# Kernel tuning notes

Hardware: AMD Instinct MI355X
Metric: run time of the kernel (lower is better)

The kernel has to match this reference:

```python
import jax, jax.numpy as jnp
import numpy as np

N_EMBED = 16384
EMBED_DIM = 256
BETA = 0.25
B, H, W = 16, 32, 32


def setup_inputs() -> dict:
    key = jax.random.key(0)
    k1, k2 = jax.random.split(key)
    z = jax.random.normal(k1, (B, EMBED_DIM, H, W), dtype=jnp.float32)
    # nn.Embedding init: uniform(-1/n_embed, 1/n_embed)
    embedding = jax.random.uniform(
        k2, (N_EMBED, EMBED_DIM), dtype=jnp.float32,
        minval=-1.0 / N_EMBED, maxval=1.0 / N_EMBED)
    return {"z": z, "embedding": embedding}


def reference(z, embedding):
    # (b, c, h, w) -> (b, h, w, c), flatten to (N, d)
    z_p = jnp.transpose(z, (0, 2, 3, 1))
    zf = z_p.reshape(-1, EMBED_DIM)  # (N, d)

    # squared distances: ||z||^2 + ||e||^2 - 2 z.e  -> (N, n_embed)
    d = (jnp.sum(zf * zf, axis=1, keepdims=True)
         + jnp.sum(embedding * embedding, axis=1)
         - 2.0 * jnp.matmul(zf, embedding.T))
    idx = jnp.argmin(d, axis=1)  # (N,)

    # one-hot encodings (returned, as in the original)
    min_encoding = jax.nn.one_hot(idx, N_EMBED, dtype=z.dtype)  # (N, n_embed)

    # codebook gather (math-equivalent to one_hot @ weight)
    z_q = jnp.take(embedding, idx, axis=0).reshape(z_p.shape)

    sg = jax.lax.stop_gradient
    loss = jnp.mean((sg(z_q) - z_p) ** 2) + BETA * jnp.mean((z_q - sg(z_p)) ** 2)

    # straight-through estimator
    z_q_st = z_p + sg(z_q - z_p)

    e_mean = jnp.mean(min_encoding, axis=0)
    perplexity = jnp.exp(-jnp.sum(e_mean * jnp.log(e_mean + 1e-10)))

    z_q_out = jnp.transpose(z_q_st, (0, 3, 1, 2))  # back to (b, c, h, w)
    return (z_q_out, loss, perplexity, min_encoding, idx[:, None])
```

## Files before the change

### kernel.cpp

```cpp
#include <hip/hip_runtime.h>
#include <math.h>

#define N_ROWS   16384
#define N_CODES  16384
#define K_DIM    256
#define HW       1024
#define N_ELEMS  4194304

#define OUT_ZQ      0
#define OUT_LOSS    4194304
#define OUT_PERP    4194305
#define OUT_ONEHOT  4194306
#define OUT_IDX     272629762

#define WS_LOSS    0
#define WS_HIST    64
#define WS_IDX     65600
#define WS_ENORM   131136
#define WS_ZNORM   196672

#define SC_ZT    0
#define SC_ZHI   16777216
#define SC_ZLO   25165824
#define SC_EHI   33554432
#define SC_BMIN  41943040
#define SC_BPACK 50331648

#define MARGIN 2.0e-4f

typedef float  floatx2 __attribute__((ext_vector_type(2)));
typedef float  f32x4   __attribute__((ext_vector_type(4)));
typedef short  bf16x8  __attribute__((ext_vector_type(8)));
typedef unsigned short u16x8 __attribute__((ext_vector_type(8)));

__device__ __forceinline__ unsigned short bf16rn(float f) {
    unsigned int x = __float_as_uint(f);
    return (unsigned short)((x + 0x7fffu + ((x >> 16) & 1u)) >> 16);
}


__global__ __launch_bounds__(256) void convert_z_kernel(
    const float* __restrict__ z, float* __restrict__ zt,
    unsigned short* __restrict__ zhi, unsigned short* __restrict__ zlo)
{
    const int tid = blockIdx.x * 256 + threadIdx.x;
    const int n  = tid & 16383;
    const int kg = tid >> 14;
    const int bimg = n >> 10, sp = n & 1023;
    const float* zp = z + (size_t)bimg * (K_DIM * HW) + (size_t)(kg * 8) * HW + sp;

    float f[8]; u16x8 hv, lv;
    #pragma unroll
    for (int j = 0; j < 8; ++j) f[j] = zp[(size_t)j * HW];
    #pragma unroll
    for (int j = 0; j < 8; ++j) {
        unsigned short h = bf16rn(f[j]);
        float fh = __uint_as_float(((unsigned int)h) << 16);
        hv[j] = h;
        lv[j] = bf16rn(f[j] - fh);
    }
    float4 a = make_float4(f[0], f[1], f[2], f[3]);
    float4 b = make_float4(f[4], f[5], f[6], f[7]);
    *(float4*)(zt + (size_t)n * 256 + kg * 8)     = a;
    *(float4*)(zt + (size_t)n * 256 + kg * 8 + 4) = b;

    const int rs = n >> 3, rowin = n & 7, kc = kg >> 3;
    const size_t stripe = (size_t)(rs * 4 + kc) * 512;
    const int inoff = rowin * 64 + (((((kg & 7) * 16)) ^ (rowin << 4)) >> 1);
    *(u16x8*)(zhi + stripe + inoff) = hv;
    *(u16x8*)(zlo + stripe + inoff) = lv;
}

__global__ __launch_bounds__(256) void convert_e_kernel(
    const float* __restrict__ emb, unsigned short* __restrict__ ehi)
{
    const int tid = blockIdx.x * 256 + threadIdx.x;
    const int kg = tid & 31;
    const int j  = tid >> 5;
    const float* ep = emb + (size_t)j * 256 + kg * 8;
    u16x8 hv;
    #pragma unroll
    for (int t = 0; t < 8; ++t) hv[t] = bf16rn(ep[t]);
    const int rs = j >> 3, rowin = j & 7, kc = kg >> 3;
    const size_t stripe = (size_t)(rs * 4 + kc) * 512;
    const int inoff = rowin * 64 + (((((kg & 7) * 16)) ^ (rowin << 4)) >> 1);
    *(u16x8*)(ehi + stripe + inoff) = hv;
}

__global__ __launch_bounds__(256) void znorm_kernel(
    const float* __restrict__ z, float* __restrict__ znorm)
{
    const int n = blockIdx.x * 256 + threadIdx.x;
    const int b = n >> 10;
    const int sp = n & 1023;
    const float* zr = z + (size_t)b * K_DIM * HW + sp;

    float h0, h1;
    {
        float r[8];
        #pragma unroll
        for (int j = 0; j < 8; ++j) {
            float v = zr[(size_t)j * HW];
            float sq = v * v; asm volatile("" : "+v"(sq));
            r[j] = sq;
        }
        for (int i = 8; i < 128; i += 8) {
            #pragma unroll
            for (int j = 0; j < 8; ++j) {
                float v = zr[(size_t)(i + j) * HW];
                float sq = v * v; asm volatile("" : "+v"(sq));
                r[j] += sq;
            }
        }
        h0 = ((r[0] + r[1]) + (r[2] + r[3])) + ((r[4] + r[5]) + (r[6] + r[7]));
    }
    {
        float r[8];
        #pragma unroll
        for (int j = 0; j < 8; ++j) {
            float v = zr[(size_t)(128 + j) * HW];
            float sq = v * v; asm volatile("" : "+v"(sq));
            r[j] = sq;
        }
        for (int i = 8; i < 128; i += 8) {
            #pragma unroll
            for (int j = 0; j < 8; ++j) {
                float v = zr[(size_t)(128 + i + j) * HW];
                float sq = v * v; asm volatile("" : "+v"(sq));
                r[j] += sq;
            }
        }
        h1 = ((r[0] + r[1]) + (r[2] + r[3])) + ((r[4] + r[5]) + (r[6] + r[7]));
    }
    znorm[n] = h0 + h1;
}

__global__ __launch_bounds__(256) void enorm_kernel(
    const float* __restrict__ emb, float* __restrict__ enorm)
{
    const int jc = blockIdx.x * 256 + threadIdx.x;
    const float* er = emb + (size_t)jc * K_DIM;

    float h0, h1;
    {
        float r[8];
        #pragma unroll
        for (int j = 0; j < 8; ++j) {
            float v = er[j];
            float sq = v * v; asm volatile("" : "+v"(sq));
            r[j] = sq;
        }
        for (int i = 8; i < 128; i += 8) {
            #pragma unroll
            for (int j = 0; j < 8; ++j) {
                float v = er[i + j];
                float sq = v * v; asm volatile("" : "+v"(sq));
                r[j] += sq;
            }
        }
        h0 = ((r[0] + r[1]) + (r[2] + r[3])) + ((r[4] + r[5]) + (r[6] + r[7]));
    }
    {
        float r[8];
        #pragma unroll
        for (int j = 0; j < 8; ++j) {
            float v = er[128 + j];
            float sq = v * v; asm volatile("" : "+v"(sq));
            r[j] = sq;
        }
        for (int i = 8; i < 128; i += 8) {
            #pragma unroll
            for (int j = 0; j < 8; ++j) {
                float v = er[128 + i + j];
                float sq = v * v; asm volatile("" : "+v"(sq));
                r[j] += sq;
            }
        }
        h1 = ((r[0] + r[1]) + (r[2] + r[3])) + ((r[4] + r[5]) + (r[6] + r[7]));
    }
    enorm[jc] = h0 + h1;
}

__global__ __launch_bounds__(512) void mfma_min_kernel(
    const unsigned short* __restrict__ zhi, const unsigned short* __restrict__ zlo,
    const unsigned short* __restrict__ ehi, const float* __restrict__ enorm,
    float* __restrict__ bmin, unsigned int* __restrict__ bpack)
{
    __shared__ unsigned short Bs[32768];
    __shared__ unsigned short As[2][16384];

    const int rb = blockIdx.x;
    const int cb = blockIdx.y;
    const int tid = threadIdx.x;
    const int wid = tid >> 6;
    const int lane = tid & 63;
    const int wr = wid >> 1;
    const int wc = wid & 1;
    const int l15 = lane & 15, l4 = lane >> 4;

    {
        const unsigned short* gb = ehi + (size_t)cb * 32768 + wid * 512 + lane * 8;
        #pragma unroll
        for (int i = 0; i < 8; ++i)
            __builtin_amdgcn_global_load_lds(
                (const __attribute__((address_space(1))) void*)(gb + i * 4096),
                (__attribute__((address_space(3))) void*)(Bs + i * 4096 + wid * 512),
                16, 0, 0);
    }
    const size_t abase = (size_t)rb * 128 * 512;
    auto stageA = [&](const unsigned short* asrc, int kc, int b) {
        #pragma unroll
        for (int i = 0; i < 4; ++i) {
            const int s = i * 8 + wid;
            const unsigned short* ga = asrc + abase + (size_t)kc * 512
                                       + (size_t)s * 2048 + lane * 8;
            __builtin_amdgcn_global_load_lds(
                (const __attribute__((address_space(1))) void*)ga,
                (__attribute__((address_space(3))) void*)(&As[b][s * 512]),
                16, 0, 0);
        }
    };

    f32x4 acc[4][4];
    #pragma unroll
    for (int mf = 0; mf < 4; ++mf)
        #pragma unroll
        for (int nf = 0; nf < 4; ++nf)
            acc[mf][nf] = (f32x4){0.f, 0.f, 0.f, 0.f};

    stageA(zhi, 0, 0);
    __syncthreads();

    for (int c = 0; c < 8; ++c) {
        const int cur = c & 1;
        if (c < 7) {
            const unsigned short* nsrc = (c + 1 < 4) ? zhi : zlo;
            stageA(nsrc, (c + 1) & 3, cur ^ 1);
        }
        const int kc = c & 3;
        #pragma unroll
        for (int sub = 0; sub < 2; ++sub) {
            bf16x8 af[4], bfr[4];
            const int kb = sub * 64 + l4 * 16;
            #pragma unroll
            for (int mf = 0; mf < 4; ++mf) {
                const int row = wr * 64 + mf * 16 + l15;
                const int off = row * 128 + (kb ^ ((row & 7) << 4));
                af[mf] = *(const bf16x8*)((const char*)&As[cur][0] + off);
            }
            #pragma unroll
            for (int nf = 0; nf < 4; ++nf) {
                const int crow = wc * 64 + nf * 16 + l15;
                const int off = ((crow >> 3) * 4 + kc) * 1024
                              + (crow & 7) * 128 + (kb ^ ((crow & 7) << 4));
                bfr[nf] = *(const bf16x8*)((const char*)Bs + off);
            }
            #pragma unroll
            for (int mf = 0; mf < 4; ++mf)
                #pragma unroll
                for (int nf = 0; nf < 4; ++nf)
                    acc[mf][nf] = __builtin_amdgcn_mfma_f32_16x16x32_bf16(
                        af[mf], bfr[nf], acc[mf][nf], 0, 0, 0);
        }
        __syncthreads();
    }

    float en[4];
    #pragma unroll
    for (int nf = 0; nf < 4; ++nf)
        en[nf] = enorm[cb * 128 + wc * 64 + nf * 16 + l15];

    float*        Vh = (float*)&As[0][0];
    unsigned int* Ih = (unsigned int*)(Vh + 512);
    unsigned int* Ch = (unsigned int*)(Ih + 512);
    float*        Gm = (float*)(Ch + 512);

    #pragma unroll
    for (int mf = 0; mf < 4; ++mf) {
        #pragma unroll
        for (int i = 0; i < 4; ++i) {
            float bv = 3.4e38f; int bc = 0x7fffffff;
            #pragma unroll
            for (int nf = 0; nf < 4; ++nf) {
                const float s = en[nf] - 2.0f * acc[mf][nf][i];
                const int col = cb * 128 + wc * 64 + nf * 16 + l15;
                if (s < bv) { bv = s; bc = col; }
            }
            #pragma unroll
            for (int off = 1; off < 16; off <<= 1) {
                const float ov = __shfl_xor(bv, off);
                const int oc = __shfl_xor(bc, off);
                if (ov < bv || (ov == bv && oc < bc)) { bv = ov; bc = oc; }
            }
            if (l15 == 0) {
                const int rr = wr * 64 + mf * 16 + l4 * 4 + i;
                Vh[wc * 256 + rr] = bv;
                Ih[wc * 256 + rr] = (unsigned int)bc;
            }
        }
    }
    __syncthreads();
    if (tid < 256) {
        const float v0 = Vh[tid], v1 = Vh[256 + tid];
        const unsigned int i0 = Ih[tid], i1 = Ih[256 + tid];
        float v; unsigned int ix;
        if (v1 < v0 || (v1 == v0 && i1 < i0)) { v = v1; ix = i1; }
        else { v = v0; ix = i0; }
        Gm[tid] = v;
        Vh[tid] = v;
        Ih[tid] = ix;
    }
    __syncthreads();
    #pragma unroll
    for (int mf = 0; mf < 4; ++mf) {
        #pragma unroll
        for (int i = 0; i < 4; ++i) {
            const int rr = wr * 64 + mf * 16 + l4 * 4 + i;
            const float thr = Gm[rr] + MARGIN;
            int cnt = 0;
            #pragma unroll
            for (int nf = 0; nf < 4; ++nf)
                cnt += (en[nf] - 2.0f * acc[mf][nf][i] <= thr) ? 1 : 0;
            #pragma unroll
            for (int off = 1; off < 16; off <<= 1) cnt += __shfl_xor(cnt, off);
            if (l15 == 0) Ch[wc * 256 + rr] = (unsigned int)cnt;
        }
    }
    __syncthreads();
    if (tid < 256) {
        unsigned int cnt = Ch[tid] + Ch[256 + tid];
        const size_t o = (size_t)(rb * 256 + tid) * 128 + cb;
        bmin[o] = Vh[tid];
        bpack[o] = (Ih[tid] << 8) | (cnt > 255u ? 255u : cnt);
    }
}

__global__ __launch_bounds__(256) void argmin_exact_kernel(
    const float* __restrict__ zt, const float* __restrict__ emb,
    const float* __restrict__ enorm, const float* __restrict__ znorm,
    const float* __restrict__ bmin, const unsigned int* __restrict__ bpack,
    int* __restrict__ idx_ws, float* __restrict__ out_idx,
    unsigned int* __restrict__ hist)
{
    __shared__ float ZL[4][256];
    const int tid = threadIdx.x, wv = tid >> 6, lane = tid & 63;
    const int n = blockIdx.x * 4 + wv;

    *(float4*)&ZL[wv][lane * 4] = ((const float4*)(zt + (size_t)n * 256))[lane];
    __syncthreads();

    const float zn = znorm[n];
    float bd = 3.4e38f; int bi = 0x7fffffff;

    const float m0 = bmin[(size_t)n * 128 + lane];
    const float m1 = bmin[(size_t)n * 128 + 64 + lane];
    float g = fminf(m0, m1);
    #pragma unroll
    for (int off = 1; off < 64; off <<= 1) g = fminf(g, __shfl_xor(g, off));
    const float thr = g + MARGIN;

    #pragma unroll
    for (int half = 0; half < 2; ++half) {
        const float bm = half ? m1 : m0;
        const unsigned int pk = bpack[(size_t)n * 128 + half * 64 + lane];
        const int cnt = (int)(pk & 255u);
        const int cand = (int)(pk >> 8);
        const bool act = (bm <= thr);
        if (act && cnt == 1) {
            const float* er = emb + (size_t)cand * 256;
            float dot = 0.f;
            for (int k = 0; k < 256; ++k) dot += ZL[wv][k] * er[k];
            const float t1 = zn + enorm[cand];
            const float d = t1 - 2.0f * dot;
            if (d < bd || (d == bd && cand < bi)) { bd = d; bi = cand; }
        }
        unsigned long long need = __ballot(act && cnt > 1);
        while (need) {
            const int c2 = __ffsll((unsigned long long)need) - 1;
            need &= need - 1;
            const int base = (half * 64 + c2) * 128;
            #pragma unroll
            for (int t = 0; t < 2; ++t) {
                const int j = base + t * 64 + lane;
                const float* er = emb + (size_t)j * 256;
                float dot = 0.f;
                for (int k = 0; k < 256; ++k) dot += ZL[wv][k] * er[k];
                const float t1 = zn + enorm[j];
                const float d = t1 - 2.0f * dot;
                if (d < bd || (d == bd && j < bi)) { bd = d; bi = j; }
            }
        }
    }
    #pragma unroll
    for (int off = 1; off < 64; off <<= 1) {
        const float od = __shfl_xor(bd, off);
        const int oi = __shfl_xor(bi, off);
        if (od < bd || (od == bd && oi < bi)) { bd = od; bi = oi; }
    }
    if (lane == 0) {
        idx_ws[n] = bi;
        out_idx[n] = (float)bi;
        atomicAdd(&hist[bi], 1u);
    }
}

__global__ __launch_bounds__(256) void gather_zq_loss_kernel(
    const float* __restrict__ z, const float* __restrict__ emb,
    const int* __restrict__ idx_ws, float* __restrict__ zq_out,
    double* __restrict__ loss_accum)
{
    const int g = blockIdx.x;
    const int wave = threadIdx.x >> 6;
    const int lane = threadIdx.x & 63;
    const int n = g * 64 + lane;
    const int b = n >> 10;
    const int sp = n & 1023;
    const int code = idx_ws[n];
    const float* erow = emb + (size_t)code * K_DIM;
    const float* zrow = z + (size_t)b * K_DIM * HW + sp;
    float* orow = zq_out + (size_t)b * K_DIM * HW + sp;

    float lsum = 0.0f;
    for (int c = wave; c < K_DIM; c += 4) {
        const float e  = erow[c];
        const float zp = zrow[(size_t)c * HW];
        orow[(size_t)c * HW] = e;
        const float d = e - zp;
        lsum += d * d;
    }
    #pragma unroll
    for (int off = 32; off; off >>= 1) lsum += __shfl_xor(lsum, off);
    __shared__ float wsum[4];
    if (lane == 0) wsum[wave] = lsum;
    __syncthreads();
    if (threadIdx.x == 0)
        atomicAdd(loss_accum, (double)(wsum[0] + wsum[1] + wsum[2] + wsum[3]));
}

__global__ __launch_bounds__(256) void onehot_fill_kernel(
    const int* __restrict__ idx_ws, float* __restrict__ out)
{
    const int r = blockIdx.x;
    const int code = idx_ws[r];
    float* row = out + (size_t)r * 16384;
    for (int s = threadIdx.x; s < 4096; s += 256) {
        if (s == 0) {
            floatx2 h = {code == 0 ? 1.f : 0.f, code == 1 ? 1.f : 0.f};
            __builtin_nontemporal_store(h, (floatx2*)row);
        }
        if (s < 4095) {
            const int cc = 2 + s * 4;
            f32x4 v = {code == cc ? 1.f : 0.f, code == cc + 1 ? 1.f : 0.f,
                       code == cc + 2 ? 1.f : 0.f, code == cc + 3 ? 1.f : 0.f};
            __builtin_nontemporal_store(v, (f32x4*)(row + cc));
        } else {
            floatx2 tpair = {code == 16382 ? 1.f : 0.f, code == 16383 ? 1.f : 0.f};
            __builtin_nontemporal_store(tpair, (floatx2*)(row + 16382));
        }
    }
}

__global__ __launch_bounds__(1024) void finalize_scalars_kernel(
    const double* __restrict__ loss_accum, const unsigned int* __restrict__ hist,
    float* __restrict__ out_scalars)
{
    const int tid = threadIdx.x;
    double s = 0.0;
    for (int j = tid; j < N_CODES; j += 1024) {
        const double p = (double)hist[j] * (1.0 / (double)N_ROWS);
        s += p * log(p + 1e-10);
    }
    #pragma unroll
    for (int off = 32; off; off >>= 1) s += __shfl_xor(s, off);
    __shared__ double sh[16];
    const int wave = tid >> 6, lane = tid & 63;
    if (lane == 0) sh[wave] = s;
    __syncthreads();
    if (tid == 0) {
        double S = 0.0;
        for (int w = 0; w < 16; ++w) S += sh[w];
        out_scalars[0] = (float)(1.25 * loss_accum[0] * (1.0 / (double)N_ELEMS));
        out_scalars[1] = (float)exp(-S);
    }
}

extern "C" void kernel_launch(void* const* d_in, const int* in_sizes, int n_in,
                              void* d_out, int out_size, void* d_ws, size_t ws_size,
                              hipStream_t stream)
{
    const float* z   = (const float*)d_in[0];
    const float* emb = (const float*)d_in[1];
    float* out = (float*)d_out;
    char* ws = (char*)d_ws;

    double*       loss_accum = (double*)(ws + WS_LOSS);
    unsigned int* hist       = (unsigned int*)(ws + WS_HIST);
    int*          idx_ws     = (int*)(ws + WS_IDX);
    float*        enorm      = (float*)(ws + WS_ENORM);
    float*        znorm      = (float*)(ws + WS_ZNORM);

    char* scb = (char*)(out + OUT_ONEHOT) + 8;
    float*          zt    = (float*)(scb + SC_ZT);
    unsigned short* zhi   = (unsigned short*)(scb + SC_ZHI);
    unsigned short* zlo   = (unsigned short*)(scb + SC_ZLO);
    unsigned short* ehi   = (unsigned short*)(scb + SC_EHI);
    float*          bminp = (float*)(scb + SC_BMIN);
    unsigned int*   bpack = (unsigned int*)(scb + SC_BPACK);

    (void)hipMemsetAsync(ws, 0, WS_ENORM, stream);

    convert_z_kernel<<<dim3(2048), dim3(256), 0, stream>>>(z, zt, zhi, zlo);
    convert_e_kernel<<<dim3(2048), dim3(256), 0, stream>>>(emb, ehi);
    znorm_kernel<<<dim3(N_ROWS / 256), dim3(256), 0, stream>>>(z, znorm);
    enorm_kernel<<<dim3(N_CODES / 256), dim3(256), 0, stream>>>(emb, enorm);

    mfma_min_kernel<<<dim3(64, 128), dim3(512), 0, stream>>>(
        zhi, zlo, ehi, enorm, bminp, bpack);

    argmin_exact_kernel<<<dim3(N_ROWS / 4), dim3(256), 0, stream>>>(
        zt, emb, enorm, znorm, bminp, bpack, idx_ws, out + OUT_IDX, hist);

    gather_zq_loss_kernel<<<dim3(N_ROWS / 64), dim3(256), 0, stream>>>(
        z, emb, idx_ws, out + OUT_ZQ, loss_accum);

    onehot_fill_kernel<<<dim3(16384), dim3(256), 0, stream>>>(
        idx_ws, out + OUT_ONEHOT);

    finalize_scalars_kernel<<<dim3(1), dim3(1024), 0, stream>>>(
        loss_accum, hist, out + OUT_LOSS);
}
```

Measured before the change: 1.979 ms.

## Drop low-bf16 z correction in screening GEMM and read A operand from global

The candidate-screening GEMM stops using a split hi/lo bf16 representation of z and uses only the hi part, which halves the MFMA work and removes the zlo conversion and its stores. To make up for the coarser screen, the margin used by the exact argmin re-check is doubled. The A operand is now loaded straight from global memory into registers instead of being double-buffered through LDS, the grid axes are swapped so column blocks vary fastest, and occupancy hints are added. A wider margin can send more candidates to the exact re-check, and unstaged global A loads may stall the MFMA pipeline.

After: 1.761 ms. 1.12x faster.

```diff
diff --git a/kernel.cpp b/kernel.cpp
--- a/kernel.cpp
+++ b/kernel.cpp
@@ -21,12 +21,11 @@
 
 #define SC_ZT    0
 #define SC_ZHI   16777216
-#define SC_ZLO   25165824
 #define SC_EHI   33554432
 #define SC_BMIN  41943040
 #define SC_BPACK 50331648
 
-#define MARGIN 2.0e-4f
+#define MARGIN 4.0e-4f
 
 typedef float  floatx2 __attribute__((ext_vector_type(2)));
 typedef float  f32x4   __attribute__((ext_vector_type(4)));
@@ -41,7 +40,7 @@
 
 __global__ __launch_bounds__(256) void convert_z_kernel(
     const float* __restrict__ z, float* __restrict__ zt,
-    unsigned short* __restrict__ zhi, unsigned short* __restrict__ zlo)
+    unsigned short* __restrict__ zhi)
 {
     const int tid = blockIdx.x * 256 + threadIdx.x;
     const int n  = tid & 16383;
@@ -49,16 +48,12 @@
     const int bimg = n >> 10, sp = n & 1023;
     const float* zp = z + (size_t)bimg * (K_DIM * HW) + (size_t)(kg * 8) * HW + sp;
 
-    float f[8]; u16x8 hv, lv;
+    float f[8]; u16x8 hv;
     #pragma unroll
     for (int j = 0; j < 8; ++j) f[j] = zp[(size_t)j * HW];
     #pragma unroll
-    for (int j = 0; j < 8; ++j) {
-        unsigned short h = bf16rn(f[j]);
-        float fh = __uint_as_float(((unsigned int)h) << 16);
-        hv[j] = h;
-        lv[j] = bf16rn(f[j] - fh);
-    }
+    for (int j = 0; j < 8; ++j) hv[j] = bf16rn(f[j]);
+
     float4 a = make_float4(f[0], f[1], f[2], f[3]);
     float4 b = make_float4(f[4], f[5], f[6], f[7]);
     *(float4*)(zt + (size_t)n * 256 + kg * 8)     = a;
@@ -66,9 +61,8 @@
 
     const int rs = n >> 3, rowin = n & 7, kc = kg >> 3;
     const size_t stripe = (size_t)(rs * 4 + kc) * 512;
-    const int inoff = rowin * 64 + (((((kg & 7) * 16)) ^ (rowin << 4)) >> 1);
+    const int inoff = rowin * 64 + ((((kg & 7) * 8)) ^ (rowin << 3));
     *(u16x8*)(zhi + stripe + inoff) = hv;
-    *(u16x8*)(zlo + stripe + inoff) = lv;
 }
 
 __global__ __launch_bounds__(256) void convert_e_kernel(
@@ -83,7 +77,7 @@
     for (int t = 0; t < 8; ++t) hv[t] = bf16rn(ep[t]);
     const int rs = j >> 3, rowin = j & 7, kc = kg >> 3;
     const size_t stripe = (size_t)(rs * 4 + kc) * 512;
-    const int inoff = rowin * 64 + (((((kg & 7) * 16)) ^ (rowin << 4)) >> 1);
+    const int inoff = rowin * 64 + ((((kg & 7) * 8)) ^ (rowin << 3));
     *(u16x8*)(ehi + stripe + inoff) = hv;
 }
 
@@ -181,16 +175,15 @@
     enorm[jc] = h0 + h1;
 }
 
-__global__ __launch_bounds__(512) void mfma_min_kernel(
-    const unsigned short* __restrict__ zhi, const unsigned short* __restrict__ zlo,
-    const unsigned short* __restrict__ ehi, const float* __restrict__ enorm,
+__global__ __launch_bounds__(512, 4) void mfma_min_kernel(
+    const unsigned short* __restrict__ zhi, const unsigned short* __restrict__ ehi,
+    const float* __restrict__ enorm,
     float* __restrict__ bmin, unsigned int* __restrict__ bpack)
 {
     __shared__ unsigned short Bs[32768];
-    __shared__ unsigned short As[2][16384];
-
-    const int rb = blockIdx.x;
-    const int cb = blockIdx.y;
+
+    const int cb = blockIdx.x;
+    const int rb = blockIdx.y;
     const int tid = threadIdx.x;
     const int wid = tid >> 6;
     const int lane = tid & 63;
@@ -207,19 +200,25 @@
                 (__attribute__((address_space(3))) void*)(Bs + i * 4096 + wid * 512),
                 16, 0, 0);
     }
-    const size_t abase = (size_t)rb * 128 * 512;
-    auto stageA = [&](const unsigned short* asrc, int kc, int b) {
-        #pragma unroll
-        for (int i = 0; i < 4; ++i) {
-            const int s = i * 8 + wid;
-            const unsigned short* ga = asrc + abase + (size_t)kc * 512
-                                       + (size_t)s * 2048 + lane * 8;
-            __builtin_amdgcn_global_load_lds(
-                (const __attribute__((address_space(1))) void*)ga,
-                (__attribute__((address_space(3))) void*)(&As[b][s * 512]),
-                16, 0, 0);
-        }
-    };
+
+    int pe[4], po[4];
+    #pragma unroll
+    for (int mf = 0; mf < 4; ++mf) {
+        const int r = rb * 256 + wr * 64 + mf * 16 + l15;
+        const int x = (r & 7) << 3;
+        const int srow = (r >> 3) * 2048 + (r & 7) * 64;
+        pe[mf] = srow + ((l4 * 8) ^ x);
+        po[mf] = srow + ((32 + l4 * 8) ^ x);
+    }
+    int qe[4], qo[4];
+    #pragma unroll
+    for (int nf = 0; nf < 4; ++nf) {
+        const int crow = wc * 64 + nf * 16 + l15;
+        const int x = (crow & 7) << 3;
+        const int srow = (crow >> 3) * 2048 + (crow & 7) * 64;
+        qe[nf] = srow + ((l4 * 8) ^ x);
+        qo[nf] = srow + ((32 + l4 * 8) ^ x);
+    }
 
     f32x4 acc[4][4];
     #pragma unroll
@@ -228,49 +227,42 @@
         for (int nf = 0; nf < 4; ++nf)
             acc[mf][nf] = (f32x4){0.f, 0.f, 0.f, 0.f};
 
-    stageA(zhi, 0, 0);
-    __syncthreads();
-
-    for (int c = 0; c < 8; ++c) {
-        const int cur = c & 1;
-        if (c < 7) {
-            const unsigned short* nsrc = (c + 1 < 4) ? zhi : zlo;
-            stageA(nsrc, (c + 1) & 3, cur ^ 1);
-        }
-        const int kc = c & 3;
-        #pragma unroll
-        for (int sub = 0; sub < 2; ++sub) {
-            bf16x8 af[4], bfr[4];
-            const int kb = sub * 64 + l4 * 16;
-            #pragma unroll
-            for (int mf = 0; mf < 4; ++mf) {
-                const int row = wr * 64 + mf * 16 + l15;
-                const int off = row * 128 + (kb ^ ((row & 7) << 4));
-                af[mf] = *(const bf16x8*)((const char*)&As[cur][0] + off);
-            }
-            #pragma unroll
-            for (int nf = 0; nf < 4; ++nf) {
-                const int crow = wc * 64 + nf * 16 + l15;
-                const int off = ((crow >> 3) * 4 + kc) * 1024
-                              + (crow & 7) * 128 + (kb ^ ((crow & 7) << 4));
-                bfr[nf] = *(const bf16x8*)((const char*)Bs + off);
-            }
+    __syncthreads();
+
+    for (int t = 0; t < 4; ++t) {
+        const int d = t * 512;
+        bf16x8 a[4];
+        #pragma unroll
+        for (int mf = 0; mf < 4; ++mf)
+            a[mf] = *(const bf16x8*)(zhi + (size_t)(pe[mf] + d));
+        #pragma unroll
+        for (int nf = 0; nf < 4; ++nf) {
+            const bf16x8 b = *(const bf16x8*)(Bs + qe[nf] + d);
             #pragma unroll
             for (int mf = 0; mf < 4; ++mf)
-                #pragma unroll
-                for (int nf = 0; nf < 4; ++nf)
-                    acc[mf][nf] = __builtin_amdgcn_mfma_f32_16x16x32_bf16(
-                        af[mf], bfr[nf], acc[mf][nf], 0, 0, 0);
-        }
-        __syncthreads();
-    }
+                acc[mf][nf] = __builtin_amdgcn_mfma_f32_16x16x32_bf16(
+                    a[mf], b, acc[mf][nf], 0, 0, 0);
+        }
+        #pragma unroll
+        for (int mf = 0; mf < 4; ++mf)
+            a[mf] = *(const bf16x8*)(zhi + (size_t)(po[mf] + d));
+        #pragma unroll
+        for (int nf = 0; nf < 4; ++nf) {
+            const bf16x8 b = *(const bf16x8*)(Bs + qo[nf] + d);
+            #pragma unroll
+            for (int mf = 0; mf < 4; ++mf)
+                acc[mf][nf] = __builtin_amdgcn_mfma_f32_16x16x32_bf16(
+                    a[mf], b, acc[mf][nf], 0, 0, 0);
+        }
+    }
+    __syncthreads();
 
     float en[4];
     #pragma unroll
     for (int nf = 0; nf < 4; ++nf)
         en[nf] = enorm[cb * 128 + wc * 64 + nf * 16 + l15];
 
-    float*        Vh = (float*)&As[0][0];
+    float*        Vh = (float*)&Bs[0];
     unsigned int* Ih = (unsigned int*)(Vh + 512);
     unsigned int* Ch = (unsigned int*)(Ih + 512);
     float*        Gm = (float*)(Ch + 512);
@@ -502,20 +494,19 @@
     char* scb = (char*)(out + OUT_ONEHOT) + 8;
     float*          zt    = (float*)(scb + SC_ZT);
     unsigned short* zhi   = (unsigned short*)(scb + SC_ZHI);
-    unsigned short* zlo   = (unsigned short*)(scb + SC_ZLO);
     unsigned short* ehi   = (unsigned short*)(scb + SC_EHI);
     float*          bminp = (float*)(scb + SC_BMIN);
     unsigned int*   bpack = (unsigned int*)(scb + SC_BPACK);
 
     (void)hipMemsetAsync(ws, 0, WS_ENORM, stream);
 
-    convert_z_kernel<<<dim3(2048), dim3(256), 0, stream>>>(z, zt, zhi, zlo);
+    convert_z_kernel<<<dim3(2048), dim3(256), 0, stream>>>(z, zt, zhi);
     convert_e_kernel<<<dim3(2048), dim3(256), 0, stream>>>(emb, ehi);
     znorm_kernel<<<dim3(N_ROWS / 256), dim3(256), 0, stream>>>(z, znorm);
     enorm_kernel<<<dim3(N_CODES / 256), dim3(256), 0, stream>>>(emb, enorm);
 
-    mfma_min_kernel<<<dim3(64, 128), dim3(512), 0, stream>>>(
-        zhi, zlo, ehi, enorm, bminp, bpack);
+    mfma_min_kernel<<<dim3(128, 64), dim3(512), 0, stream>>>(
+        zhi, ehi, enorm, bminp, bpack);
 
     argmin_exact_kernel<<<dim3(N_ROWS / 4), dim3(256), 0, stream>>>(
         zt, emb, enorm, znorm, bminp, bpack, idx_ws, out + OUT_IDX, hist);
```
